# Kernel tuning notes

Measured on AMD Instinct MI355X. Metric: run time of the kernel, lower is better.

The kernel has to match this reference:

```python
import jax, jax.numpy as jnp
import numpy as np

GRID_LON = 17  # idx = lat*17 + lon in original code


def setup_inputs() -> dict:
    key = jax.random.key(0)
    ks = jax.random.split(key, 16)
    B, S, L = 512, 256, 64
    DIM_RHO, DIM_C, HID = 256, 128, 512
    N_LAT, N_LON = 17, GRID_LON

    rho = jax.random.normal(ks[0], (B, S, DIM_RHO), dtype=jnp.float32)
    c = jax.random.normal(ks[1], (1, DIM_C, N_LAT, N_LON), dtype=jnp.float32)
    w = jax.random.uniform(ks[2], (B, S), dtype=jnp.float32, minval=1e-3, maxval=1.0)
    l = jax.random.uniform(ks[3], (B,), dtype=jnp.float32, minval=0.1, maxval=10.0)
    roads = jax.random.randint(ks[4], (B, L), 0, N_LAT * N_LON)
    lon_idx = jax.random.randint(ks[5], (B, L), 0, N_LON)
    lat_idx = jax.random.randint(ks[6], (B, L), 0, N_LAT)

    sc = lambda fan_in: 1.0 / np.sqrt(fan_in)
    # f2: MLP(128, 256, 128) with selu
    f2_W1 = jax.random.uniform(ks[7], (DIM_C, 256), jnp.float32, -sc(DIM_C), sc(DIM_C))
    f2_b1 = jnp.zeros((256,), jnp.float32)
    f2_W2 = jax.random.uniform(ks[8], (256, DIM_C), jnp.float32, -sc(256), sc(256))
    f2_b2 = jnp.zeros((DIM_C,), jnp.float32)
    # f: MLP2(dim_rho + dim_c, hidden, 1) with selu (use_selu=True)
    fin = DIM_RHO + DIM_C
    f_W1 = jax.random.uniform(ks[9], (fin, HID), jnp.float32, -sc(fin), sc(fin))
    f_b1 = jnp.zeros((HID,), jnp.float32)
    f_W21 = jax.random.uniform(ks[10], (HID, 1), jnp.float32, -sc(HID), sc(HID))
    f_b21 = jnp.zeros((1,), jnp.float32)
    f_W22 = jax.random.uniform(ks[11], (HID, 1), jnp.float32, -sc(HID), sc(HID))
    f_b22 = jnp.zeros((1,), jnp.float32)

    return dict(rho=rho, c=c, w=w, l=l, roads=roads, lon_idx=lon_idx,
                lat_idx=lat_idx, f2_W1=f2_W1, f2_b1=f2_b1, f2_W2=f2_W2,
                f2_b2=f2_b2, f_W1=f_W1, f_b1=f_b1, f_W21=f_W21, f_b21=f_b21,
                f_W22=f_W22, f_b22=f_b22)


def reference(rho, c, w, l, roads, lon_idx, lat_idx,
              f2_W1, f2_b1, f2_W2, f2_b2,
              f_W1, f_b1, f_W21, f_b21, f_W22, f_b22):
    # c: (1, dim_c, n_lat, n_lon) -> (n_lat*n_lon, dim_c)
    c3 = jnp.squeeze(c, 0)                       # (dim_c, n_lat, n_lon)
    c_flat = jnp.transpose(c3, (1, 2, 0)).reshape(-1, c3.shape[0])  # (cells, dim_c)

    # ragged gather-mean, vectorized: (B, L) cell indices -> (B, dim_c)
    idx = lat_idx * GRID_LON + lon_idx           # (B, L)
    c_traj = jnp.mean(c_flat[idx], axis=1)       # (B, dim_c)

    # f2: selu MLP (dropout inactive / eval mode)
    h = jax.nn.selu(c_traj @ f2_W1 + f2_b1)
    c_tr = h @ f2_W2 + f2_b2                     # (B, dim_c)

    # broadcast over seq and concat with rho
    S = rho.shape[1]
    c_exp = jnp.broadcast_to(c_tr[:, None, :], (rho.shape[0], S, c_tr.shape[-1]))
    x = jnp.concatenate([rho, c_exp], axis=2)    # (B, S, dim_rho + dim_c)

    # f (MLP2, selu since use_selu=True)
    h1 = jax.nn.selu(x @ f_W1 + f_b1)            # (B, S, hidden)
    logm = (h1 @ f_W21 + f_b21)[..., 0]          # (B, S)
    logv = (h1 @ f_W22 + f_b22)[..., 0]          # (B, S)

    logw = jnp.log(w)
    logm_agg = jax.nn.logsumexp(logm + logw, axis=1)       # (B,)
    logv_agg = jax.nn.logsumexp(logv + 2.0 * logw, axis=1) # (B,)
    logl = jnp.log(l)
    log_mu = logl - logm_agg
    log_lambda = logl - 3.0 * logm_agg - logv_agg
    return (log_mu, log_lambda)
```

## Files before the change

kernel.cpp:

```cpp
#include <hip/hip_runtime.h>
#include <hip/hip_bf16.h>

typedef short bf16x8 __attribute__((ext_vector_type(8)));
typedef float f32x4 __attribute__((ext_vector_type(4)));

__device__ __forceinline__ short f2bf(float f) {
    union { float f; unsigned u; } v; v.f = f;
    unsigned r = (v.u + 0x7FFFu + ((v.u >> 16) & 1u)) >> 16;
    return (short)r;
}

__device__ __forceinline__ float selu_f(float x) {
    const float scale = 1.0507009873554805f;
    const float sa = 1.0507009873554805f * 1.6732632423543772f;
    return x > 0.f ? scale * x : sa * (__expf(x) - 1.f);
}

__global__ void __launch_bounds__(512) prep_cbias_kernel(
    const float* __restrict__ c, const int* __restrict__ lat_idx,
    const int* __restrict__ lon_idx,
    const float* __restrict__ f2W1, const float* __restrict__ f2b1,
    const float* __restrict__ f2W2, const float* __restrict__ f2b2,
    const float* __restrict__ fW1, const float* __restrict__ fb1,
    float* __restrict__ cbias)
{
    __shared__ int cells[64];
    __shared__ float ctraj[128];
    __shared__ float hbuf[256];
    __shared__ float ctrf[128];
    const int b = blockIdx.x;
    const int t = threadIdx.x;

    if (t < 64) cells[t] = lat_idx[b * 64 + t] * 17 + lon_idx[b * 64 + t];
    __syncthreads();

    if (t < 128) {
        float s = 0.f;
        #pragma unroll 8
        for (int j = 0; j < 64; ++j) s += c[t * 289 + cells[j]];
        ctraj[t] = s * (1.f / 64.f);
    }
    __syncthreads();

    if (t < 256) {
        float acc = f2b1[t];
        #pragma unroll 8
        for (int i = 0; i < 128; ++i) acc += ctraj[i] * f2W1[i * 256 + t];
        hbuf[t] = selu_f(acc);
    }
    __syncthreads();

    if (t < 128) {
        float acc = f2b2[t];
        #pragma unroll 8
        for (int i = 0; i < 256; ++i) acc += hbuf[i] * f2W2[i * 128 + t];
        ctrf[t] = acc;
    }
    __syncthreads();

    float acc = fb1[t];
    #pragma unroll 8
    for (int i = 0; i < 128; ++i) acc += ctrf[i] * fW1[(256 + i) * 512 + t];
    cbias[b * 512 + t] = acc;
}

__global__ void __launch_bounds__(256) build_w1img_kernel(
    const float* __restrict__ fW1, short* __restrict__ img)
{
    int I = blockIdx.x * 256 + threadIdx.x;
    int e = I & 7;
    int lane = (I >> 3) & 63;
    int cg = (I >> 9) & 31;
    int kc = I >> 14;
    int col = cg * 16 + (lane & 15);
    int k = kc * 32 + ((lane >> 4) << 3) + e;
    img[I] = f2bf(fW1[k * 512 + col]);
}

__global__ void __launch_bounds__(512, 4) fused_gemm_kernel(
    const float* __restrict__ rho, const short* __restrict__ w1img,
    const float* __restrict__ cbias, const float* __restrict__ fw21,
    const float* __restrict__ fw22,
    float* __restrict__ plm, float* __restrict__ plv)
{
    __shared__ __align__(16) char smA[32768];
    __shared__ float redM[8][64];
    __shared__ float redV[8][64];

    const int tid  = threadIdx.x;
    const int lane = tid & 63;
    const int w    = tid >> 6;
    const int l15  = lane & 15;
    const int hi   = lane >> 4;

    const int b  = blockIdx.x >> 2;
    const int s0 = (blockIdx.x & 2) << 5 | (blockIdx.x & 1) << 6;
    const int s0v = (blockIdx.x & 3) << 6;

    {
        const float* rbase = rho + (size_t)(b * 256 + s0v) * 256;
        #pragma unroll
        for (int i = 0; i < 4; ++i) {
            int slot = i * 512 + tid;
            int kc = slot >> 8;
            int rem = slot & 255;
            int rg = rem >> 6;
            int ls = rem & 63;
            int row = rg * 16 + (ls & 15);
            int k0 = kc * 32 + ((ls >> 4) << 3);
            const float* src = rbase + (size_t)row * 256 + k0;
            float4 f0 = *(const float4*)(src);
            float4 f1 = *(const float4*)(src + 4);
            bf16x8 h;
            h[0] = f2bf(f0.x); h[1] = f2bf(f0.y); h[2] = f2bf(f0.z); h[3] = f2bf(f0.w);
            h[4] = f2bf(f1.x); h[5] = f2bf(f1.y); h[6] = f2bf(f1.z); h[7] = f2bf(f1.w);
            *(bf16x8*)(smA + slot * 16) = h;
        }
    }
    __syncthreads();

    f32x4 acc[4][4];
    #pragma unroll
    for (int rf = 0; rf < 4; ++rf)
        #pragma unroll
        for (int cf = 0; cf < 4; ++cf)
            acc[rf][cf] = (f32x4){0.f, 0.f, 0.f, 0.f};

    const char* bp = (const char*)w1img + w * 4096 + lane * 16;

    bf16x8 bN[4];
    #pragma unroll
    for (int cf = 0; cf < 4; ++cf)
        bN[cf] = *(const bf16x8*)(bp + cf * 1024);

    #pragma unroll
    for (int kc = 0; kc < 8; ++kc) {
        bf16x8 bC[4];
        #pragma unroll
        for (int cf = 0; cf < 4; ++cf) bC[cf] = bN[cf];
        if (kc < 7) {
            #pragma unroll
            for (int cf = 0; cf < 4; ++cf)
                bN[cf] = *(const bf16x8*)(bp + (size_t)(kc + 1) * 32768 + cf * 1024);
        }
        bf16x8 aF[4];
        #pragma unroll
        for (int rf = 0; rf < 4; ++rf)
            aF[rf] = *(const bf16x8*)(smA + ((kc * 4 + rf) * 64 + lane) * 16);
        #pragma unroll
        for (int rf = 0; rf < 4; ++rf)
            #pragma unroll
            for (int cf = 0; cf < 4; ++cf)
                acc[rf][cf] = __builtin_amdgcn_mfma_f32_16x16x32_bf16(
                    aF[rf], bC[cf], acc[rf][cf], 0, 0, 0);
    }

    float cb[4], w21r[4], w22r[4];
    #pragma unroll
    for (int cf = 0; cf < 4; ++cf) {
        int col = w * 64 + cf * 16 + l15;
        cb[cf]   = cbias[b * 512 + col];
        w21r[cf] = fw21[col];
        w22r[cf] = fw22[col];
    }

    #pragma unroll
    for (int rf = 0; rf < 4; ++rf)
        #pragma unroll
        for (int q = 0; q < 4; ++q) {
            float m = 0.f, v = 0.f;
            #pragma unroll
            for (int cf = 0; cf < 4; ++cf) {
                float s_ = selu_f(acc[rf][cf][q] + cb[cf]);
                m += s_ * w21r[cf];
                v += s_ * w22r[cf];
            }
            #pragma unroll
            for (int d = 1; d < 16; d <<= 1) {
                m += __shfl_xor(m, d);
                v += __shfl_xor(v, d);
            }
            if (l15 == 0) {
                int row = rf * 16 + hi * 4 + q;
                redM[w][row] = m;
                redV[w][row] = v;
            }
        }

    __syncthreads();
    size_t obase = (size_t)b * 256 + s0v;
    if (tid < 64) {
        float s = 0.f;
        #pragma unroll
        for (int j = 0; j < 8; ++j) s += redM[j][tid];
        plm[obase + tid] = s;
    } else if (tid < 128) {
        int rr = tid - 64;
        float s = 0.f;
        #pragma unroll
        for (int j = 0; j < 8; ++j) s += redV[j][rr];
        plv[obase + rr] = s;
    }
}

__global__ void __launch_bounds__(64) finalize_kernel(
    const float* __restrict__ plm, const float* __restrict__ plv,
    const float* __restrict__ w, const float* __restrict__ l,
    const float* __restrict__ b21p, const float* __restrict__ b22p,
    float* __restrict__ out)
{
    const int b = blockIdx.x;
    const int lane = threadIdx.x;
    const float b21 = b21p[0], b22 = b22p[0];

    float a1[4], a2[4];
    float m1 = -1e30f, m2 = -1e30f;
    #pragma unroll
    for (int i = 0; i < 4; ++i) {
        int s = i * 64 + lane;
        float lw = logf(w[b * 256 + s]);
        a1[i] = plm[b * 256 + s] + b21 + lw;
        a2[i] = plv[b * 256 + s] + b22 + 2.f * lw;
        m1 = fmaxf(m1, a1[i]);
        m2 = fmaxf(m2, a2[i]);
    }
    #pragma unroll
    for (int m = 1; m < 64; m <<= 1) {
        m1 = fmaxf(m1, __shfl_xor(m1, m));
        m2 = fmaxf(m2, __shfl_xor(m2, m));
    }
    float s1 = 0.f, s2 = 0.f;
    #pragma unroll
    for (int i = 0; i < 4; ++i) {
        s1 += expf(a1[i] - m1);
        s2 += expf(a2[i] - m2);
    }
    #pragma unroll
    for (int m = 1; m < 64; m <<= 1) {
        s1 += __shfl_xor(s1, m);
        s2 += __shfl_xor(s2, m);
    }
    if (lane == 0) {
        float lm_agg = m1 + logf(s1);
        float lv_agg = m2 + logf(s2);
        float logl = logf(l[b]);
        out[b]       = logl - lm_agg;
        out[512 + b] = logl - 3.f * lm_agg - lv_agg;
    }
}

extern "C" void kernel_launch(void* const* d_in, const int* in_sizes, int n_in,
                              void* d_out, int out_size, void* d_ws, size_t ws_size,
                              hipStream_t stream) {
    const float* rho     = (const float*)d_in[0];
    const float* c       = (const float*)d_in[1];
    const float* w       = (const float*)d_in[2];
    const float* l       = (const float*)d_in[3];
    const int*   lon_idx = (const int*)d_in[5];
    const int*   lat_idx = (const int*)d_in[6];
    const float* f2W1    = (const float*)d_in[7];
    const float* f2b1    = (const float*)d_in[8];
    const float* f2W2    = (const float*)d_in[9];
    const float* f2b2    = (const float*)d_in[10];
    const float* fW1     = (const float*)d_in[11];
    const float* fb1     = (const float*)d_in[12];
    const float* fW21    = (const float*)d_in[13];
    const float* fb21    = (const float*)d_in[14];
    const float* fW22    = (const float*)d_in[15];
    const float* fb22    = (const float*)d_in[16];
    float* out = (float*)d_out;

    char* ws = (char*)d_ws;
    float* cbias  = (float*)(ws);
    short* w1img  = (short*)(ws + 1048576);
    float* plm    = (float*)(ws + 1310720);
    float* plv    = (float*)(ws + 1835008);

    prep_cbias_kernel<<<512, 512, 0, stream>>>(c, lat_idx, lon_idx,
                                               f2W1, f2b1, f2W2, f2b2,
                                               fW1, fb1, cbias);
    build_w1img_kernel<<<512, 256, 0, stream>>>(fW1, w1img);
    fused_gemm_kernel<<<2048, 512, 0, stream>>>(rho, w1img, cbias, fW21, fW22,
                                                plm, plv);
    finalize_kernel<<<512, 64, 0, stream>>>(plm, plv, w, l, fb21, fb22, out);
}
```

Measured before the change: 106.0 us.

## Transpose GEMM operands and reduce SELU output against W21/W22 with MFMA

The main GEMM swaps its MFMA operands so each lane holds four consecutive hidden columns for one sequence row. The epilogue then applies SELU, packs the results to fp16 and multiplies them by a prebuilt fp16 weight matrix using a 16x16x16 MFMA. That MFMA computes the logm and logv dot products directly, replacing the per-element FMAs and the 4-step shuffle reductions. This adds a small kernel that builds the padded weight matrix, and it costs fp16 precision on the SELU activations and weights.

Result: faster. 98.43 us (-7.1%).

```diff
diff --git a/kernel.cpp b/kernel.cpp
--- a/kernel.cpp
+++ b/kernel.cpp
@@ -3,6 +3,7 @@
 
 typedef short bf16x8 __attribute__((ext_vector_type(8)));
 typedef float f32x4 __attribute__((ext_vector_type(4)));
+typedef _Float16 half4 __attribute__((ext_vector_type(4)));
 
 __device__ __forceinline__ short f2bf(float f) {
     union { float f; unsigned u; } v; v.f = f;
@@ -77,10 +78,23 @@
     img[I] = f2bf(fW1[k * 512 + col]);
 }
 
+__global__ void __launch_bounds__(256) build_wvec_kernel(
+    const float* __restrict__ fW21, const float* __restrict__ fW22,
+    _Float16* __restrict__ wvec)
+{
+    int I = blockIdx.x * 256 + threadIdx.x;
+    int e = I & 3;
+    int lane = (I >> 2) & 63;
+    int nc = I >> 8;
+    int l15 = lane & 15, hi = lane >> 4;
+    int n = nc * 16 + hi * 4 + e;
+    float v = (l15 == 0) ? fW21[n] : (l15 == 1 ? fW22[n] : 0.f);
+    wvec[I] = (_Float16)v;
+}
+
 __global__ void __launch_bounds__(512, 4) fused_gemm_kernel(
     const float* __restrict__ rho, const short* __restrict__ w1img,
-    const float* __restrict__ cbias, const float* __restrict__ fw21,
-    const float* __restrict__ fw22,
+    const float* __restrict__ cbias, const _Float16* __restrict__ wvec,
     float* __restrict__ plm, float* __restrict__ plv)
 {
     __shared__ __align__(16) char smA[32768];
@@ -93,8 +107,7 @@
     const int l15  = lane & 15;
     const int hi   = lane >> 4;
 
-    const int b  = blockIdx.x >> 2;
-    const int s0 = (blockIdx.x & 2) << 5 | (blockIdx.x & 1) << 6;
+    const int b   = blockIdx.x >> 2;
     const int s0v = (blockIdx.x & 3) << 6;
 
     {
@@ -121,71 +134,68 @@
 
     f32x4 acc[4][4];
     #pragma unroll
-    for (int rf = 0; rf < 4; ++rf)
-        #pragma unroll
-        for (int cf = 0; cf < 4; ++cf)
-            acc[rf][cf] = (f32x4){0.f, 0.f, 0.f, 0.f};
+    for (int nf = 0; nf < 4; ++nf)
+        #pragma unroll
+        for (int sf = 0; sf < 4; ++sf)
+            acc[nf][sf] = (f32x4){0.f, 0.f, 0.f, 0.f};
 
     const char* bp = (const char*)w1img + w * 4096 + lane * 16;
 
     bf16x8 bN[4];
     #pragma unroll
-    for (int cf = 0; cf < 4; ++cf)
-        bN[cf] = *(const bf16x8*)(bp + cf * 1024);
+    for (int nf = 0; nf < 4; ++nf)
+        bN[nf] = *(const bf16x8*)(bp + nf * 1024);
 
     #pragma unroll
     for (int kc = 0; kc < 8; ++kc) {
         bf16x8 bC[4];
         #pragma unroll
-        for (int cf = 0; cf < 4; ++cf) bC[cf] = bN[cf];
+        for (int nf = 0; nf < 4; ++nf) bC[nf] = bN[nf];
         if (kc < 7) {
             #pragma unroll
-            for (int cf = 0; cf < 4; ++cf)
-                bN[cf] = *(const bf16x8*)(bp + (size_t)(kc + 1) * 32768 + cf * 1024);
+            for (int nf = 0; nf < 4; ++nf)
+                bN[nf] = *(const bf16x8*)(bp + (size_t)(kc + 1) * 32768 + nf * 1024);
         }
         bf16x8 aF[4];
         #pragma unroll
-        for (int rf = 0; rf < 4; ++rf)
-            aF[rf] = *(const bf16x8*)(smA + ((kc * 4 + rf) * 64 + lane) * 16);
-        #pragma unroll
-        for (int rf = 0; rf < 4; ++rf)
+        for (int sf = 0; sf < 4; ++sf)
+            aF[sf] = *(const bf16x8*)(smA + ((kc * 4 + sf) * 64 + lane) * 16);
+        #pragma unroll
+        for (int nf = 0; nf < 4; ++nf)
             #pragma unroll
-            for (int cf = 0; cf < 4; ++cf)
-                acc[rf][cf] = __builtin_amdgcn_mfma_f32_16x16x32_bf16(
-                    aF[rf], bC[cf], acc[rf][cf], 0, 0, 0);
-    }
-
-    float cb[4], w21r[4], w22r[4];
-    #pragma unroll
-    for (int cf = 0; cf < 4; ++cf) {
-        int col = w * 64 + cf * 16 + l15;
-        cb[cf]   = cbias[b * 512 + col];
-        w21r[cf] = fw21[col];
-        w22r[cf] = fw22[col];
-    }
-
-    #pragma unroll
-    for (int rf = 0; rf < 4; ++rf)
-        #pragma unroll
-        for (int q = 0; q < 4; ++q) {
-            float m = 0.f, v = 0.f;
+            for (int sf = 0; sf < 4; ++sf)
+                acc[nf][sf] = __builtin_amdgcn_mfma_f32_16x16x32_bf16(
+                    bC[nf], aF[sf], acc[nf][sf], 0, 0, 0);
+    }
+
+    f32x4 rd[4];
+    #pragma unroll
+    for (int sf = 0; sf < 4; ++sf) rd[sf] = (f32x4){0.f, 0.f, 0.f, 0.f};
+
+    const int wn = w * 64;
+    #pragma unroll
+    for (int nf = 0; nf < 4; ++nf) {
+        f32x4 cbf = *(const f32x4*)(cbias + b * 512 + wn + nf * 16 + hi * 4);
+        half4 wv = *(const half4*)(wvec + (size_t)(w * 4 + nf) * 256 + lane * 4);
+        #pragma unroll
+        for (int sf = 0; sf < 4; ++sf) {
+            half4 pa;
             #pragma unroll
-            for (int cf = 0; cf < 4; ++cf) {
-                float s_ = selu_f(acc[rf][cf][q] + cb[cf]);
-                m += s_ * w21r[cf];
-                v += s_ * w22r[cf];
-            }
-            #pragma unroll
-            for (int d = 1; d < 16; d <<= 1) {
-                m += __shfl_xor(m, d);
-                v += __shfl_xor(v, d);
-            }
-            if (l15 == 0) {
-                int row = rf * 16 + hi * 4 + q;
-                redM[w][row] = m;
-                redV[w][row] = v;
-            }
+            for (int q = 0; q < 4; ++q)
+                pa[q] = (_Float16)selu_f(acc[nf][sf][q] + cbf[q]);
+            rd[sf] = __builtin_amdgcn_mfma_f32_16x16x16f16(pa, wv, rd[sf], 0, 0, 0);
         }
+    }
+
+    if (l15 == 0) {
+        #pragma unroll
+        for (int sf = 0; sf < 4; ++sf)
+            *(f32x4*)&redM[w][sf * 16 + hi * 4] = rd[sf];
+    } else if (l15 == 1) {
+        #pragma unroll
+        for (int sf = 0; sf < 4; ++sf)
+            *(f32x4*)&redV[w][sf * 16 + hi * 4] = rd[sf];
+    }
 
     __syncthreads();
     size_t obase = (size_t)b * 256 + s0v;
@@ -271,16 +281,18 @@
     float* out = (float*)d_out;
 
     char* ws = (char*)d_ws;
-    float* cbias  = (float*)(ws);
-    short* w1img  = (short*)(ws + 1048576);
-    float* plm    = (float*)(ws + 1310720);
-    float* plv    = (float*)(ws + 1835008);
+    float*     cbias = (float*)(ws);
+    short*     w1img = (short*)(ws + 1048576);
+    float*     plm   = (float*)(ws + 1310720);
+    float*     plv   = (float*)(ws + 1835008);
+    _Float16*  wvec  = (_Float16*)(ws + 2359296);
 
     prep_cbias_kernel<<<512, 512, 0, stream>>>(c, lat_idx, lon_idx,
                                                f2W1, f2b1, f2W2, f2b2,
                                                fW1, fb1, cbias);
     build_w1img_kernel<<<512, 256, 0, stream>>>(fW1, w1img);
-    fused_gemm_kernel<<<2048, 512, 0, stream>>>(rho, w1img, cbias, fW21, fW22,
+    build_wvec_kernel<<<32, 256, 0, stream>>>(fW21, fW22, wvec);
+    fused_gemm_kernel<<<2048, 512, 0, stream>>>(rho, w1img, cbias, wvec,
                                                 plm, plv);
     finalize_kernel<<<512, 64, 0, stream>>>(plm, plv, w, l, fb21, fb22, out);
 }
```
